# Kernel optimization log

Measured on AMD Instinct MI355X. Metric: run time of the kernel, lower is better.

The kernel has to match this reference:

```python
import jax, jax.numpy as jnp
import numpy as np

BN_EPS = 1e-5


def setup_inputs() -> dict:
    key = jax.random.key(0)
    k1, k2, k3 = jax.random.split(key, 3)
    B, IN, H, C = 65536, 784, 1024, 10
    x = jax.random.normal(k1, (B, IN), dtype=jnp.float32)
    # Kaiming-ish real-valued latent weights
    w1 = jax.random.normal(k2, (H, IN), dtype=jnp.float32) * 0.03
    w2 = jax.random.normal(k3, (C, H), dtype=jnp.float32) * 0.03
    gamma = jnp.ones((H,), dtype=jnp.float32)
    beta = jnp.zeros((H,), dtype=jnp.float32)
    return {"x": x, "w1": w1, "w2": w2, "gamma": gamma, "beta": beta}


def _bin_weight(w):
    # XNOR-Net weight binarization: per-output-row alpha * sign(w)
    alpha = jnp.mean(jnp.abs(w), axis=1, keepdims=True)  # [out, 1]
    return alpha * jnp.sign(w)


def reference(x, w1, w2, gamma, beta):
    x = x.reshape(x.shape[0], -1)                      # [B, 784]
    h = x @ _bin_weight(w1).T                          # [B, 1024]
    # BatchNorm1d, training mode: batch mean / biased variance
    mu = jnp.mean(h, axis=0)
    var = jnp.mean(jnp.square(h - mu), axis=0)
    h = gamma * (h - mu) * jax.lax.rsqrt(var + BN_EPS) + beta
    a = jnp.sign(h)                                    # binarized activation
    out = a @ _bin_weight(w2).T                        # [B, 10]
    return out
```

## Files before the change

### kernel.cpp

```cpp
#include <hip/hip_runtime.h>
#include <hip/hip_fp16.h>

#define BATCH   65536
#define IN_DIM  784
#define KH      800
#define NSTEP   25
#define H_DIM   1024
#define C_DIM   10
#define BN_EPS  1e-5f
#define SLOTH   16384

typedef _Float16 half8 __attribute__((ext_vector_type(8)));
typedef float    f32x4 __attribute__((ext_vector_type(4)));

#if defined(__has_builtin)
#if __has_builtin(__builtin_amdgcn_global_load_lds)
#define HAVE_ASYNC 1
#endif
#endif
#ifndef HAVE_ASYNC
#define HAVE_ASYNC 0
#endif

__device__ __forceinline__ void stage16(const void* g, void* ldsBase, int lane) {
#if HAVE_ASYNC
  __builtin_amdgcn_global_load_lds((const __attribute__((address_space(1))) void*)g,
                                   (__attribute__((address_space(3))) void*)ldsBase,
                                   16, 0, 0);
#else
  *(half8*)((_Float16*)ldsBase + lane * 8) = *(const half8*)((const _Float16*)g + lane * 8);
#endif
}

__global__ __launch_bounds__(256) void prep_w(const float* __restrict__ w1,
                                              const float* __restrict__ w2,
                                              float* __restrict__ alpha1,
                                              _Float16* __restrict__ S2,
                                              _Float16* __restrict__ S2W,
                                              float* __restrict__ A2P,
                                              float* __restrict__ colz) {
  __shared__ float red[4];
  const int tid = threadIdx.x, lane = tid & 63, wave = tid >> 6;
  const int j = blockIdx.x;
  if (j < H_DIM) {
    const float* wr = w1 + (long)j * IN_DIM;
    float s = 0.f;
    for (int k = tid; k < IN_DIM; k += 256) s += fabsf(wr[k]);
#pragma unroll
    for (int off = 32; off > 0; off >>= 1) s += __shfl_xor(s, off, 64);
    if (lane == 0) red[wave] = s;
    __syncthreads();
    if (tid == 0) alpha1[j] = (red[0] + red[1] + red[2] + red[3]) * (1.f / IN_DIM);
    _Float16* dr = S2 + (long)j * KH;
    for (int k = tid; k < KH; k += 256) {
      const float v = (k < IN_DIM) ? wr[k] : 0.f;
      dr[k] = (_Float16)((v > 0.f) ? 1.f : ((v < 0.f) ? -1.f : 0.f));
    }
  } else if (j < H_DIM + C_DIM) {
    const int c = j - H_DIM;
    const float* wr = w2 + (long)c * H_DIM;
    float s = 0.f;
    for (int k = tid; k < H_DIM; k += 256) s += fabsf(wr[k]);
#pragma unroll
    for (int off = 32; off > 0; off >>= 1) s += __shfl_xor(s, off, 64);
    if (lane == 0) red[wave] = s;
    __syncthreads();
    if (tid == 0) A2P[c] = (red[0] + red[1] + red[2] + red[3]) * (1.f / H_DIM);
    for (int k = tid; k < H_DIM; k += 256) {
      const float v = wr[k];
      S2W[(long)c * H_DIM + k] = (_Float16)((v > 0.f) ? 1.f : ((v < 0.f) ? -1.f : 0.f));
    }
  } else {
    for (int k = tid; k < 2 * H_DIM; k += 256) colz[k] = 0.f;
    for (int k = tid; k < 6 * H_DIM; k += 256) S2W[10 * H_DIM + k] = (_Float16)0.f;
    if (tid < 6) A2P[10 + tid] = 0.f;
  }
}

__global__ __launch_bounds__(512, 4) void gemm1(const float* __restrict__ x,
                                                const _Float16* __restrict__ S2,
                                                const float* __restrict__ alpha1,
                                                float* __restrict__ H,
                                                float* __restrict__ colsum,
                                                float* __restrict__ colsumsq) {
  __shared__ _Float16 lds[2 * SLOTH];
  const int tid  = threadIdx.x;
  const int lane = tid & 63;
  const int w    = tid >> 6;
  const int wr   = w >> 2;
  const int wc   = w & 3;

  const int b     = blockIdx.x;
  const int xcd   = b & 7;
  const int local = b >> 3;
  const long m0   = (long)(xcd * 64 + (local >> 2)) * 128;
  const int  n0   = (local & 3) * 256;

  const int rowS = tid >> 2;
  const int q    = tid & 3;
  const float* xp = x + (m0 + rowS) * (long)IN_DIM;
  const int cq = (q ^ ((rowS >> 1) & 3)) * 8;
  const int aw = rowS * 32;

  const int c8 = ((lane & 3) ^ ((lane >> 3) & 3)) * 8;
  const _Float16* bG = S2 + (long)(n0 + w * 32 + (lane >> 2)) * KH + c8;
  const int ldsW0 = (w * 32) * 32;
  const int ldsW1 = (w * 32 + 16) * 32;

  const int fr = lane & 15;
  const int kc = lane >> 4;
  const int cp = (kc ^ ((fr >> 1) & 3)) * 8;
  const int aoff = (wr * 64 + fr) * 32 + cp;
  const int boff = (wc * 64 + fr) * 32 + cp;

  f32x4 acc[4][4] = {};

#define ALOAD(R0, R1, KB) do {                                               \
    if (((KB) + q * 8) <= (IN_DIM - 8)) {                                    \
      const float* src = xp + (KB) + q * 8;                                  \
      (R0) = *(const f32x4*)(src);                                           \
      (R1) = *(const f32x4*)(src + 4);                                       \
    } else { (R0) = f32x4{}; (R1) = f32x4{}; }                               \
  } while (0)

#define CONV_WRITE(R0, R1, PW, KB) do {                                      \
    half8 hh = {}, hl = {};                                                  \
    if (((KB) + q * 8) <= (IN_DIM - 8)) {                                    \
      _Pragma("unroll")                                                      \
      for (int i = 0; i < 8; ++i) {                                          \
        const float f = (i < 4) ? (R0)[i] : (R1)[i & 3];                     \
        const _Float16 h = (_Float16)f;                                      \
        hh[i] = h; hl[i] = (_Float16)(f - (float)h);                         \
      }                                                                      \
    }                                                                        \
    *(half8*)((PW) + aw + cq) = hh;                                          \
    *(half8*)((PW) + 4096 + aw + cq) = hl;                                   \
  } while (0)

  stage16(bG + 0,           lds + 8192 + ldsW0, lane);
  stage16(bG + 16 * KH + 0, lds + 8192 + ldsW1, lane);
  {
    f32x4 r0, r1;
    ALOAD(r0, r1, 0);
    asm volatile("s_waitcnt vmcnt(0)" ::: "memory");
    CONV_WRITE(r0, r1, (&lds[0]), 0);
  }

  for (int t = 0; t < NSTEP; ++t) {
    _Float16* Scur = &lds[(t & 1) * SLOTH];
    _Float16* Pw   = &lds[((t + 1) & 1) * SLOTH];
    const int kb = ((t + 1 < NSTEP) ? (t + 1) : (NSTEP - 1)) * 32;

    asm volatile("s_waitcnt lgkmcnt(0)" ::: "memory");
    __builtin_amdgcn_s_barrier();
    asm volatile("" ::: "memory");

    stage16(bG + kb,           Pw + 8192 + ldsW0, lane);
    stage16(bG + 16 * KH + kb, Pw + 8192 + ldsW1, lane);
    f32x4 r0, r1;
    ALOAD(r0, r1, kb);

    half8 af[4], bf[4];
#pragma unroll
    for (int ni = 0; ni < 4; ++ni) bf[ni] = *(const half8*)&Scur[8192 + boff + ni * 512];
#pragma unroll
    for (int mi = 0; mi < 4; ++mi) af[mi] = *(const half8*)&Scur[aoff + mi * 512];
    __builtin_amdgcn_s_setprio(1);
#pragma unroll
    for (int mi = 0; mi < 4; ++mi)
#pragma unroll
      for (int ni = 0; ni < 4; ++ni)
        acc[mi][ni] = __builtin_amdgcn_mfma_f32_16x16x32_f16(af[mi], bf[ni], acc[mi][ni], 0, 0, 0);
    __builtin_amdgcn_s_setprio(0);
#pragma unroll
    for (int mi = 0; mi < 4; ++mi) af[mi] = *(const half8*)&Scur[4096 + aoff + mi * 512];
    __builtin_amdgcn_s_setprio(1);
#pragma unroll
    for (int mi = 0; mi < 4; ++mi)
#pragma unroll
      for (int ni = 0; ni < 4; ++ni)
        acc[mi][ni] = __builtin_amdgcn_mfma_f32_16x16x32_f16(af[mi], bf[ni], acc[mi][ni], 0, 0, 0);
    __builtin_amdgcn_s_setprio(0);

    asm volatile("s_waitcnt vmcnt(0)" ::: "memory");
    CONV_WRITE(r0, r1, Pw, kb);
  }

  asm volatile("s_waitcnt vmcnt(0)" ::: "memory");

  const int rq = (lane >> 4) * 4;
#pragma unroll
  for (int ni = 0; ni < 4; ++ni) {
    const int col = n0 + wc * 64 + ni * 16 + fr;
    const float a1 = alpha1[col];
    float s = 0.f, qq = 0.f;
#pragma unroll
    for (int mi = 0; mi < 4; ++mi) {
#pragma unroll
      for (int r = 0; r < 4; ++r) {
        const long row = m0 + wr * 64 + mi * 16 + rq + r;
        const float v = acc[mi][ni][r] * a1;
        H[row * H_DIM + col] = v;
        s += v;
        qq += v * v;
      }
    }
    s += __shfl_xor(s, 16, 64);
    s += __shfl_xor(s, 32, 64);
    qq += __shfl_xor(qq, 16, 64);
    qq += __shfl_xor(qq, 32, 64);
    if ((lane >> 4) == 0) {
      atomicAdd(&colsum[col], s);
      atomicAdd(&colsumsq[col], qq);
    }
  }
#undef ALOAD
#undef CONV_WRITE
}

__global__ __launch_bounds__(256) void final_k(const float* __restrict__ H,
                                               const float* __restrict__ colsum,
                                               const float* __restrict__ colsumsq,
                                               const float* __restrict__ gamma,
                                               const float* __restrict__ beta,
                                               const _Float16* __restrict__ S2W,
                                               const float* __restrict__ A2P,
                                               float* __restrict__ out) {
  __shared__ _Float16 bs[16 * H_DIM];
  __shared__ float cs[H_DIM], ts[H_DIM];
  const int tid = threadIdx.x, lane = tid & 63, wave = tid >> 6;

  {
    const int j = tid * 4;
    const f32x4 s  = *(const f32x4*)&colsum[j];
    const f32x4 q  = *(const f32x4*)&colsumsq[j];
    const f32x4 g  = *(const f32x4*)&gamma[j];
    const f32x4 bt = *(const f32x4*)&beta[j];
    f32x4 c, t;
#pragma unroll
    for (int i = 0; i < 4; ++i) {
      const float mu  = s[i] * (1.f / BATCH);
      const float var = q[i] * (1.f / BATCH) - mu * mu;
      c[i] = g[i] * rsqrtf(var + BN_EPS);
      t[i] = bt[i] - c[i] * mu;
    }
    *(f32x4*)&cs[j] = c;
    *(f32x4*)&ts[j] = t;
  }
  for (int i = tid; i < 2048; i += 256) {
    const int oc = i >> 7, cc = i & 127;
    *(half8*)&bs[oc * H_DIM + ((cc ^ (oc & 7)) << 3)] = *(const half8*)&S2W[oc * H_DIM + (cc << 3)];
  }
  __syncthreads();

  const int lr = lane & 15, lg = lane >> 4;
  const float alf = A2P[lr];
  const long r0 = ((long)blockIdx.x * 4 + wave) * 16;
  const float* hp = H + (r0 + lr) * H_DIM + lg * 8;

  f32x4 acc = {};
#pragma unroll 4
  for (int ks = 0; ks < 32; ++ks) {
    const f32x4 h0 = *(const f32x4*)(hp + ks * 32);
    const f32x4 h1 = *(const f32x4*)(hp + ks * 32 + 4);
    const int jb = ks * 32 + lg * 8;
    const f32x4 c0v = *(const f32x4*)&cs[jb];
    const f32x4 c1v = *(const f32x4*)&cs[jb + 4];
    const f32x4 t0v = *(const f32x4*)&ts[jb];
    const f32x4 t1v = *(const f32x4*)&ts[jb + 4];
    half8 afr;
#pragma unroll
    for (int i = 0; i < 4; ++i) {
      const float hv = h0[i] * c0v[i] + t0v[i];
      afr[i] = (_Float16)((hv > 0.f) ? 1.f : ((hv < 0.f) ? -1.f : 0.f));
    }
#pragma unroll
    for (int i = 0; i < 4; ++i) {
      const float hv = h1[i] * c1v[i] + t1v[i];
      afr[4 + i] = (_Float16)((hv > 0.f) ? 1.f : ((hv < 0.f) ? -1.f : 0.f));
    }
    const int cc = (ks * 4 + lg) ^ (lr & 7);
    const half8 bfr = *(const half8*)&bs[lr * H_DIM + cc * 8];
    acc = __builtin_amdgcn_mfma_f32_16x16x32_f16(afr, bfr, acc, 0, 0, 0);
  }

  __syncthreads();
  float* outs = (float*)bs;
  if (lr < C_DIM) {
#pragma unroll
    for (int r = 0; r < 4; ++r)
      outs[(wave * 16 + lg * 4 + r) * C_DIM + lr] = acc[r] * alf;
  }
  __syncthreads();
  if (tid < 160)
    *(f32x4*)&out[(long)blockIdx.x * 640 + tid * 4] = *(const f32x4*)&outs[tid * 4];
}

extern "C" void kernel_launch(void* const* d_in, const int* in_sizes, int n_in,
                              void* d_out, int out_size, void* d_ws, size_t ws_size,
                              hipStream_t stream) {
  const float* x     = (const float*)d_in[0];
  const float* w1    = (const float*)d_in[1];
  const float* w2    = (const float*)d_in[2];
  const float* gamma = (const float*)d_in[3];
  const float* beta  = (const float*)d_in[4];
  float* out = (float*)d_out;

  char* ws = (char*)d_ws;
  float*    H      = (float*)   (ws + 0);
  _Float16* S2     = (_Float16*)(ws + 268435456LL);
  _Float16* S2W    = (_Float16*)(ws + 270073856LL);
  float*    ALPHA1 = (float*)   (ws + 270106624LL);
  float*    A2P    = (float*)   (ws + 270110720LL);
  float*    COLS   = (float*)   (ws + 270110976LL);
  float*    COLQ   = (float*)   (ws + 270115072LL);

  prep_w<<<H_DIM + C_DIM + 1, 256, 0, stream>>>(w1, w2, ALPHA1, S2, S2W, A2P, COLS);
  gemm1<<<2048, 512, 0, stream>>>(x, S2, ALPHA1, H, COLS, COLQ);
  final_k<<<BATCH / 64, 256, 0, stream>>>(H, COLS, COLQ, gamma, beta, S2W, A2P, out);
}
```

Baseline: 536.1 us.

## Triple-buffer B tile in LDS to prefetch weights two steps ahead

Splits the LDS staging into separate A (double-buffered) and B (triple-buffered) regions. The B weight tiles are now fetched asynchronously two k-steps ahead, and the end-of-step wait becomes vmcnt(2), so only the A register loads must land before conversion. This is meant to hide global-to-LDS latency for the weights instead of draining all outstanding loads every step. LDS use grows from 64KB to 56KB-equivalent layout (2*8192+3*8192 halves = 80KB), which may reduce occupancy, and the vmcnt ordering relies on the A loads being issued before the B stages.

```diff
diff --git a/kernel.cpp b/kernel.cpp
--- a/kernel.cpp
+++ b/kernel.cpp
@@ -8,7 +8,9 @@
 #define H_DIM   1024
 #define C_DIM   10
 #define BN_EPS  1e-5f
-#define SLOTH   16384
+#define ASLOT   8192
+#define BBASE   16384
+#define BSLOT   8192
 
 typedef _Float16 half8 __attribute__((ext_vector_type(8)));
 typedef float    f32x4 __attribute__((ext_vector_type(4)));
@@ -83,7 +85,7 @@
                                                 float* __restrict__ H,
                                                 float* __restrict__ colsum,
                                                 float* __restrict__ colsumsq) {
-  __shared__ _Float16 lds[2 * SLOTH];
+  __shared__ _Float16 lds[2 * ASLOT + 3 * BSLOT];
   const int tid  = threadIdx.x;
   const int lane = tid & 63;
   const int w    = tid >> 6;
@@ -137,8 +139,10 @@
     *(half8*)((PW) + 4096 + aw + cq) = hl;                                   \
   } while (0)
 
-  stage16(bG + 0,           lds + 8192 + ldsW0, lane);
-  stage16(bG + 16 * KH + 0, lds + 8192 + ldsW1, lane);
+  stage16(bG + 0,            lds + BBASE + ldsW0, lane);
+  stage16(bG + 16 * KH + 0,  lds + BBASE + ldsW1, lane);
+  stage16(bG + 32,           lds + BBASE + BSLOT + ldsW0, lane);
+  stage16(bG + 16 * KH + 32, lds + BBASE + BSLOT + ldsW1, lane);
   {
     f32x4 r0, r1;
     ALOAD(r0, r1, 0);
@@ -147,24 +151,28 @@
   }
 
   for (int t = 0; t < NSTEP; ++t) {
-    _Float16* Scur = &lds[(t & 1) * SLOTH];
-    _Float16* Pw   = &lds[((t + 1) & 1) * SLOTH];
-    const int kb = ((t + 1 < NSTEP) ? (t + 1) : (NSTEP - 1)) * 32;
+    _Float16* Acur = &lds[(t & 1) * ASLOT];
+    _Float16* Apre = &lds[((t + 1) & 1) * ASLOT];
+    _Float16* Bcur = &lds[BBASE + (t % 3) * BSLOT];
+    _Float16* Bpre = &lds[BBASE + ((t + 2) % 3) * BSLOT];
+    const int kbA = ((t + 1 < NSTEP) ? (t + 1) : (NSTEP - 1)) * 32;
+    const int kbB = ((t + 2 < NSTEP) ? (t + 2) : (NSTEP - 1)) * 32;
 
     asm volatile("s_waitcnt lgkmcnt(0)" ::: "memory");
     __builtin_amdgcn_s_barrier();
     asm volatile("" ::: "memory");
 
-    stage16(bG + kb,           Pw + 8192 + ldsW0, lane);
-    stage16(bG + 16 * KH + kb, Pw + 8192 + ldsW1, lane);
     f32x4 r0, r1;
-    ALOAD(r0, r1, kb);
+    ALOAD(r0, r1, kbA);
+    asm volatile("" ::: "memory");
+    stage16(bG + kbB,           Bpre + ldsW0, lane);
+    stage16(bG + 16 * KH + kbB, Bpre + ldsW1, lane);
 
     half8 af[4], bf[4];
 #pragma unroll
-    for (int ni = 0; ni < 4; ++ni) bf[ni] = *(const half8*)&Scur[8192 + boff + ni * 512];
-#pragma unroll
-    for (int mi = 0; mi < 4; ++mi) af[mi] = *(const half8*)&Scur[aoff + mi * 512];
+    for (int ni = 0; ni < 4; ++ni) bf[ni] = *(const half8*)&Bcur[boff + ni * 512];
+#pragma unroll
+    for (int mi = 0; mi < 4; ++mi) af[mi] = *(const half8*)&Acur[aoff + mi * 512];
     __builtin_amdgcn_s_setprio(1);
 #pragma unroll
     for (int mi = 0; mi < 4; ++mi)
@@ -173,7 +181,7 @@
         acc[mi][ni] = __builtin_amdgcn_mfma_f32_16x16x32_f16(af[mi], bf[ni], acc[mi][ni], 0, 0, 0);
     __builtin_amdgcn_s_setprio(0);
 #pragma unroll
-    for (int mi = 0; mi < 4; ++mi) af[mi] = *(const half8*)&Scur[4096 + aoff + mi * 512];
+    for (int mi = 0; mi < 4; ++mi) af[mi] = *(const half8*)&Acur[4096 + aoff + mi * 512];
     __builtin_amdgcn_s_setprio(1);
 #pragma unroll
     for (int mi = 0; mi < 4; ++mi)
@@ -182,8 +190,8 @@
         acc[mi][ni] = __builtin_amdgcn_mfma_f32_16x16x32_f16(af[mi], bf[ni], acc[mi][ni], 0, 0, 0);
     __builtin_amdgcn_s_setprio(0);
 
-    asm volatile("s_waitcnt vmcnt(0)" ::: "memory");
-    CONV_WRITE(r0, r1, Pw, kb);
+    asm volatile("s_waitcnt vmcnt(2)" ::: "memory");
+    CONV_WRITE(r0, r1, Apre, kbA);
   }
 
   asm volatile("s_waitcnt vmcnt(0)" ::: "memory");
```

Result: slower. 610.9 us (+14.0%).
